# Performance work log

Hardware: AMD Instinct MI355X
Metric: run time of the kernel (lower is better)

## Reference

```python
import jax, jax.numpy as jnp
import numpy as np

B, P, D = 256, 256, 514          # batch, num_patches (16^2), model_dim
H, HD = 8, 64                    # n_heads, head_dim ((D-2)//H)
SH = 256                         # shared_hidden = head_mlp_hidden_dims[0]
HH = 256                         # per-head hidden (head_mlp_hidden_dims[1])
DFF = 2048                       # ffn hidden
LH = 2 * SH                      # lat_modulator hidden = shared_hidden*2
LD = D - 2                       # learnable_dim

def gelu(x):
    return jax.nn.gelu(x, approximate=False)  # torch nn.GELU default is exact erf

def setup_inputs() -> dict:
    key = jax.random.key(0)
    ks = jax.random.split(key, 16)
    s = 0.02
    x = jax.random.normal(ks[0], (B, P, D), dtype=jnp.float32)
    # shared spatial layer: Linear(P -> SH), torch weight layout [out, in]
    Ws = jax.random.normal(ks[1], (SH, P), dtype=jnp.float32) * s
    bs = jax.random.normal(ks[2], (SH,), dtype=jnp.float32) * s
    # lat modulator: Linear(2 -> LH), GELU, Linear(LH -> 2*SH) with special init
    LW1 = jax.random.normal(ks[3], (LH, 2), dtype=jnp.float32) * s
    Lb1 = jax.random.normal(ks[4], (LH,), dtype=jnp.float32) * s
    LW2 = jnp.zeros((2 * SH, LH), dtype=jnp.float32)  # zeroed per module init
    Lb2 = jnp.concatenate([jnp.ones((SH,), jnp.float32), jnp.zeros((SH,), jnp.float32)])
    # per-head processing: Linear(SH->HH), GELU, Linear(HH->P), stacked over heads
    HW1 = jax.random.normal(ks[5], (H, HH, SH), dtype=jnp.float32) * s
    Hb1 = jax.random.normal(ks[6], (H, HH), dtype=jnp.float32) * s
    HW2 = jax.random.normal(ks[7], (H, P, HH), dtype=jnp.float32) * s
    Hb2 = jax.random.normal(ks[8], (H, P), dtype=jnp.float32) * s
    # ffn: Linear(D -> DFF) with last-2 input cols zeroed, GELU, Linear(DFF -> LD)
    FW1 = jax.random.normal(ks[9], (DFF, D), dtype=jnp.float32) * s
    FW1 = FW1.at[:, -2:].set(0.0)
    Fb1 = jax.random.normal(ks[10], (DFF,), dtype=jnp.float32) * s
    FW2 = jax.random.normal(ks[11], (LD, DFF), dtype=jnp.float32) * s
    Fb2 = jax.random.normal(ks[12], (LD,), dtype=jnp.float32) * s
    return dict(x=x, Ws=Ws, bs=bs, LW1=LW1, Lb1=Lb1, LW2=LW2, Lb2=Lb2,
                HW1=HW1, Hb1=Hb1, HW2=HW2, Hb2=Hb2,
                FW1=FW1, Fb1=Fb1, FW2=FW2, Fb2=Fb2)

def reference(x, Ws, bs, LW1, Lb1, LW2, Lb2, HW1, Hb1, HW2, Hb2, FW1, Fb1, FW2, Fb2):
    central = P // 2
    sc_central = x[:, central, -2:]          # [B, 2]
    sc_all = x[:, :, -2:]                    # [B, P, 2]
    x_learn = x[:, :, :-2]                   # [B, P, LD]
    x_res = x_learn
    # all heads at once: [B, P, H, HD] -> [B, H, HD, P]
    xh = x_learn.reshape(B, P, H, HD).transpose(0, 2, 3, 1)
    shared = jnp.einsum('bhdp,op->bhdo', xh, Ws) + bs   # [B, H, HD, SH]
    # FiLM params (loop-invariant in original, hoisted here)
    mod = gelu(sc_central @ LW1.T + Lb1) @ LW2.T + Lb2  # [B, 2*SH]
    gamma = mod[:, :SH][:, None, None, :]
    beta = mod[:, SH:][:, None, None, :]
    shared = shared * gamma + beta
    # per-head MLPs as grouped GEMMs
    h = gelu(jnp.einsum('bhdo,hko->bhdk', shared, HW1) + Hb1[None, :, None, :])
    out = jnp.einsum('bhdk,hpk->bhdp', h, HW2) + Hb2[None, :, None, :]  # [B,H,HD,P]
    x_learn = out.transpose(0, 3, 1, 2).reshape(B, P, LD) + x_res
    x_full = jnp.concatenate([x_learn, sc_all], axis=-1)  # [B, P, D]
    f = gelu(x_full @ FW1.T + Fb1) @ FW2.T + Fb2          # [B, P, LD]
    x_learn = f + x_learn
    return jnp.concatenate([x_learn, sc_all], axis=-1)
```

## Files before the change

kernel.cpp:

```cpp
#include <hip/hip_runtime.h>
#include <math.h>

typedef __attribute__((ext_vector_type(8))) __bf16 bf16x8;
typedef __attribute__((ext_vector_type(4))) float f32x4;
typedef __attribute__((ext_vector_type(2))) float f32x2;

#define DEV __device__ __forceinline__

typedef __attribute__((address_space(3))) unsigned int lds_u32;
typedef __attribute__((address_space(1))) unsigned int glb_u32;

DEV unsigned short f2bf(float f) {
    unsigned int u = __builtin_bit_cast(unsigned int, f);
    u += 0x7FFFu + ((u >> 16) & 1u);
    return (unsigned short)(u >> 16);
}
DEV float bf2f(unsigned short u) {
    unsigned int v = (unsigned int)u << 16;
    return __builtin_bit_cast(float, v);
}
DEV unsigned int pack2(float a, float b) {
    return (unsigned int)f2bf(a) | ((unsigned int)f2bf(b) << 16);
}
DEV float gelu_exact(float v) {
    return 0.5f * v * (1.0f + erff(v * 0.70710678118654752f));
}
DEV float gelu_fast(float x) {
    float z = 1.5957691216f * x + 0.0713548163f * x * x * x;
    float e = __expf(-z);
    return x * __builtin_amdgcn_rcpf(1.0f + e);
}

__global__ void cast_bf16_kernel(const float* __restrict__ src,
                                 unsigned short* __restrict__ dst, int n) {
    int i = blockIdx.x * 256 + threadIdx.x;
    if (i < n) dst[i] = f2bf(src[i]);
}

__global__ void cast_fw1_kernel(const float* __restrict__ src,
                                unsigned short* __restrict__ dst) {
    int i = blockIdx.x * 256 + threadIdx.x;
    if (i < 2048 * 512) {
        int row = i >> 9, k = i & 511;
        dst[i] = f2bf(src[row * 514 + k]);
    }
}

__global__ void gb_kernel(const float* __restrict__ x,
                          const float* __restrict__ LW1, const float* __restrict__ Lb1,
                          const float* __restrict__ LW2, const float* __restrict__ Lb2,
                          float* __restrict__ gb) {
    __shared__ float t[8][512];
    const int b0 = blockIdx.x * 8, tid = threadIdx.x;
    for (int idx = tid; idx < 8 * 512; idx += 256) {
        int bb = idx >> 9, j = idx & 511;
        float s0 = x[((size_t)(b0 + bb) * 256 + 128) * 514 + 512];
        float s1 = x[((size_t)(b0 + bb) * 256 + 128) * 514 + 513];
        t[bb][j] = gelu_exact(LW1[j * 2] * s0 + LW1[j * 2 + 1] * s1 + Lb1[j]);
    }
    __syncthreads();
    const int i = tid;
    float a0[8], a1[8];
    float l0 = Lb2[i], l1 = Lb2[i + 256];
    #pragma unroll
    for (int bb = 0; bb < 8; ++bb) { a0[bb] = l0; a1[bb] = l1; }
    for (int j = 0; j < 512; ++j) {
        float w0 = LW2[(size_t)i * 512 + j];
        float w1 = LW2[(size_t)(i + 256) * 512 + j];
        #pragma unroll
        for (int bb = 0; bb < 8; ++bb) {
            a0[bb] += w0 * t[bb][j];
            a1[bb] += w1 * t[bb][j];
        }
    }
    #pragma unroll
    for (int bb = 0; bb < 8; ++bb) {
        gb[(size_t)(b0 + bb) * 512 + i] = a0[bb];
        gb[(size_t)(b0 + bb) * 512 + i + 256] = a1[bb];
    }
}

__global__ void sc_copy_kernel(const float* __restrict__ x, float* __restrict__ out,
                               float* __restrict__ scbuf) {
    size_t idx = (size_t)blockIdx.x * 256 + threadIdx.x;
    size_t off = idx * 514 + 512;
    f32x2 v = *(const f32x2*)(x + off);
    *(f32x2*)(out + off) = v;
    *(f32x2*)(scbuf + idx * 2) = v;
}

#define MPAD 264

__global__ __launch_bounds__(256, 2) void mixer_kernel(
    const float* __restrict__ x, const float* __restrict__ bs,
    const float* __restrict__ Hb1, const float* __restrict__ Hb2,
    const unsigned short* __restrict__ Wsb,
    const unsigned short* __restrict__ HW1b,
    const unsigned short* __restrict__ HW2b,
    const float* __restrict__ gb,
    unsigned short* __restrict__ Xb) {
    __shared__ __attribute__((aligned(16))) char smem[33792 + 34816];
    unsigned short* XT = (unsigned short*)smem;
    unsigned short* S = (unsigned short*)(smem + 33792);
    unsigned short* ST = S;

    const int bid = blockIdx.x;
    const int b = bid >> 3;
    const int h = bid & 7;
    const int tid = threadIdx.x;
    const int lane = tid & 63;
    const int w = tid >> 6;
    const int l15 = lane & 15;
    const int l4 = lane >> 4;

    {
        const int c = lane;
        const float* xp = x + ((size_t)b * 256) * 514 + (size_t)h * 64 + c;
        float v[64];
        #pragma unroll
        for (int p = 0; p < 64; ++p)
            v[p] = xp[(size_t)(w * 64 + p) * 514];
        #pragma unroll
        for (int g = 0; g < 8; ++g) {
            uint4 pk;
            pk.x = pack2(v[g * 8 + 0], v[g * 8 + 1]);
            pk.y = pack2(v[g * 8 + 2], v[g * 8 + 3]);
            pk.z = pack2(v[g * 8 + 4], v[g * 8 + 5]);
            pk.w = pack2(v[g * 8 + 6], v[g * 8 + 7]);
            *(uint4*)&XT[c * MPAD + w * 64 + g * 8] = pk;
        }
    }
    __syncthreads();

    f32x4 acc[4][4];

    #pragma unroll
    for (int mt = 0; mt < 4; ++mt)
        #pragma unroll
        for (int nt = 0; nt < 4; ++nt) acc[mt][nt] = 0.f;
    {
        const unsigned short* Wp = Wsb;
        bf16x8 bn1[4], bn2[4];
        #pragma unroll
        for (int nt = 0; nt < 4; ++nt) {
            bn1[nt] = *(const bf16x8*)(Wp + (size_t)(w * 64 + nt * 16 + l15) * 256 + 0 * 32 + l4 * 8);
            bn2[nt] = *(const bf16x8*)(Wp + (size_t)(w * 64 + nt * 16 + l15) * 256 + 1 * 32 + l4 * 8);
        }
        for (int kc = 0; kc < 8; ++kc) {
            bf16x8 bcur[4];
            #pragma unroll
            for (int nt = 0; nt < 4; ++nt) { bcur[nt] = bn1[nt]; bn1[nt] = bn2[nt]; }
            if (kc < 6) {
                #pragma unroll
                for (int nt = 0; nt < 4; ++nt)
                    bn2[nt] = *(const bf16x8*)(Wp + (size_t)(w * 64 + nt * 16 + l15) * 256 + (kc + 2) * 32 + l4 * 8);
            }
            #pragma unroll
            for (int mt = 0; mt < 4; ++mt) {
                bf16x8 afr = *(const bf16x8*)&XT[(mt * 16 + l15) * MPAD + kc * 32 + l4 * 8];
                #pragma unroll
                for (int nt = 0; nt < 4; ++nt)
                    acc[mt][nt] = __builtin_amdgcn_mfma_f32_16x16x32_bf16(afr, bcur[nt], acc[mt][nt], 0, 0, 0);
            }
        }
    }
    #pragma unroll
    for (int nt = 0; nt < 4; ++nt) {
        int o = w * 64 + nt * 16 + l15;
        float bsv = bs[o];
        float g = gb[(size_t)b * 512 + o];
        float be = gb[(size_t)b * 512 + 256 + o];
        #pragma unroll
        for (int mt = 0; mt < 4; ++mt)
            #pragma unroll
            for (int r = 0; r < 4; ++r) {
                int c = mt * 16 + l4 * 4 + r;
                S[c * MPAD + o] = f2bf((acc[mt][nt][r] + bsv) * g + be);
            }
    }
    __syncthreads();

    const unsigned short* W2p = HW1b + (size_t)h * 65536;
    #pragma unroll
    for (int mt = 0; mt < 4; ++mt)
        #pragma unroll
        for (int nt = 0; nt < 4; ++nt) acc[mt][nt] = 0.f;
    {
        bf16x8 bn1[4], bn2[4];
        #pragma unroll
        for (int nt = 0; nt < 4; ++nt) {
            bn1[nt] = *(const bf16x8*)(W2p + (size_t)(w * 64 + nt * 16 + l15) * 256 + 0 * 32 + l4 * 8);
            bn2[nt] = *(const bf16x8*)(W2p + (size_t)(w * 64 + nt * 16 + l15) * 256 + 1 * 32 + l4 * 8);
        }
        for (int kc = 0; kc < 8; ++kc) {
            bf16x8 bcur[4];
            #pragma unroll
            for (int nt = 0; nt < 4; ++nt) { bcur[nt] = bn1[nt]; bn1[nt] = bn2[nt]; }
            if (kc < 6) {
                #pragma unroll
                for (int nt = 0; nt < 4; ++nt)
                    bn2[nt] = *(const bf16x8*)(W2p + (size_t)(w * 64 + nt * 16 + l15) * 256 + (kc + 2) * 32 + l4 * 8);
            }
            #pragma unroll
            for (int mt = 0; mt < 4; ++mt) {
                bf16x8 afr = *(const bf16x8*)&S[(mt * 16 + l15) * MPAD + kc * 32 + l4 * 8];
                #pragma unroll
                for (int nt = 0; nt < 4; ++nt)
                    acc[mt][nt] = __builtin_amdgcn_mfma_f32_16x16x32_bf16(afr, bcur[nt], acc[mt][nt], 0, 0, 0);
            }
        }
    }
    __syncthreads();
    #pragma unroll
    for (int nt = 0; nt < 4; ++nt) {
        int kk = w * 64 + nt * 16 + l15;
        float hb = Hb1[(size_t)h * 256 + kk];
        #pragma unroll
        for (int mt = 0; mt < 4; ++mt)
            #pragma unroll
            for (int r = 0; r < 4; ++r) {
                int c = mt * 16 + l4 * 4 + r;
                S[c * MPAD + kk] = f2bf(gelu_fast(acc[mt][nt][r] + hb));
            }
    }
    __syncthreads();

    const unsigned short* W3p = HW2b + (size_t)h * 65536;
    #pragma unroll
    for (int mt = 0; mt < 4; ++mt)
        #pragma unroll
        for (int nt = 0; nt < 4; ++nt) acc[mt][nt] = 0.f;
    {
        bf16x8 bn1[4], bn2[4];
        #pragma unroll
        for (int nt = 0; nt < 4; ++nt) {
            bn1[nt] = *(const bf16x8*)(W3p + (size_t)(w * 64 + nt * 16 + l15) * 256 + 0 * 32 + l4 * 8);
            bn2[nt] = *(const bf16x8*)(W3p + (size_t)(w * 64 + nt * 16 + l15) * 256 + 1 * 32 + l4 * 8);
        }
        for (int kc = 0; kc < 8; ++kc) {
            bf16x8 bcur[4];
            #pragma unroll
            for (int nt = 0; nt < 4; ++nt) { bcur[nt] = bn1[nt]; bn1[nt] = bn2[nt]; }
            if (kc < 6) {
                #pragma unroll
                for (int nt = 0; nt < 4; ++nt)
                    bn2[nt] = *(const bf16x8*)(W3p + (size_t)(w * 64 + nt * 16 + l15) * 256 + (kc + 2) * 32 + l4 * 8);
            }
            #pragma unroll
            for (int mt = 0; mt < 4; ++mt) {
                bf16x8 afr = *(const bf16x8*)&S[(mt * 16 + l15) * MPAD + kc * 32 + l4 * 8];
                #pragma unroll
                for (int nt = 0; nt < 4; ++nt)
                    acc[mt][nt] = __builtin_amdgcn_mfma_f32_16x16x32_bf16(afr, bcur[nt], acc[mt][nt], 0, 0, 0);
            }
        }
    }
    __syncthreads();

    #pragma unroll
    for (int nt = 0; nt < 4; ++nt) {
        int p = w * 64 + nt * 16 + l15;
        float hb = Hb2[(size_t)h * 256 + p];
        #pragma unroll
        for (int mt = 0; mt < 4; ++mt) {
            int c0 = mt * 16 + l4 * 4;
            ushort4 uv;
            uv.x = f2bf(acc[mt][nt][0] + hb + bf2f(XT[(c0 + 0) * MPAD + p]));
            uv.y = f2bf(acc[mt][nt][1] + hb + bf2f(XT[(c0 + 1) * MPAD + p]));
            uv.z = f2bf(acc[mt][nt][2] + hb + bf2f(XT[(c0 + 2) * MPAD + p]));
            uv.w = f2bf(acc[mt][nt][3] + hb + bf2f(XT[(c0 + 3) * MPAD + p]));
            *(ushort4*)(ST + p * 68 + c0) = uv;
        }
    }
    __syncthreads();

    #pragma unroll
    for (int s = 0; s < 16; ++s) {
        int row = s * 16 + w * 4 + l4;
        ushort4 u = *(const ushort4*)(ST + row * 68 + l15 * 4);
        *(ushort4*)(Xb + ((size_t)(b * 256 + row)) * 512 + h * 64 + l15 * 4) = u;
    }
}

DEV void stage_m97(const unsigned short* g, size_t gstride, int row0, int k0,
                   char* lbuf, int tid) {
    const int slot = tid & 7;
    const int r8 = (tid >> 3) & 7;
    const int wv = tid >> 6;
    const int swz = (slot ^ r8) * 16;
    #pragma unroll
    for (int i = 0; i < 4; ++i) {
        int chunk = i * 4 + wv;
        int row = chunk * 8 + r8;
        const char* src = (const char*)(g + (size_t)(row0 + row) * gstride + k0) + swz;
        __builtin_amdgcn_global_load_lds((const glb_u32*)src,
                                         (lds_u32*)(lbuf + chunk * 1024), 16, 0, 0);
    }
}

DEV void gemm_loop97(const unsigned short* A, size_t sA,
                     const unsigned short* B, size_t sB,
                     int m0, int n0, int NT,
                     char* smem, int tid, f32x4 (&acc)[4][4]) {
    const int lane = tid & 63;
    const int w = tid >> 6;
    const int l15 = lane & 15, l4 = lane >> 4;
    const int wm = w >> 1, wn = w & 1;

    for (int t = 0; t < NT; ++t) {
        stage_m97(A, sA, m0, t * 64, smem, tid);
        stage_m97(B, sB, n0, t * 64, smem + 16384, tid);
        __syncthreads();
        #pragma unroll
        for (int kk = 0; kk < 2; ++kk) {
            bf16x8 af[4], bf[4];
            #pragma unroll
            for (int mf = 0; mf < 4; ++mf) {
                int row = wm * 64 + mf * 16 + l15;
                af[mf] = *(const bf16x8*)(smem + row * 128 + ((kk * 64 + l4 * 16) ^ ((row & 7) << 4)));
            }
            #pragma unroll
            for (int nf = 0; nf < 4; ++nf) {
                int row = wn * 64 + nf * 16 + l15;
                bf[nf] = *(const bf16x8*)(smem + 16384 + row * 128 + ((kk * 64 + l4 * 16) ^ ((row & 7) << 4)));
            }
            #pragma unroll
            for (int mf = 0; mf < 4; ++mf)
                #pragma unroll
                for (int nf = 0; nf < 4; ++nf)
                    acc[mf][nf] = __builtin_amdgcn_mfma_f32_16x16x32_bf16(
                        af[mf], bf[nf], acc[mf][nf], 0, 0, 0);
        }
        __syncthreads();
    }
}

__global__ __launch_bounds__(256, 3) void gemm1_kernel(
    const unsigned short* __restrict__ A,
    const unsigned short* __restrict__ B,
    const float* __restrict__ Fb1,
    const float* __restrict__ FW1,
    const float* __restrict__ scbuf,
    long pass_m0,
    unsigned short* __restrict__ G) {
    __shared__ __attribute__((aligned(16))) char smem[34816];

    const int nwg = gridDim.x;
    const int cpx = nwg >> 3;
    const int bid = (blockIdx.x & 7) * cpx + (blockIdx.x >> 3);
    const int m0 = (bid >> 4) * 128;
    const int n0 = (bid & 15) * 128;
    const int tid = threadIdx.x;
    const int lane = tid & 63;
    const int w = tid >> 6;
    const int l15 = lane & 15;
    const int l4 = lane >> 4;
    const int wm = w >> 1, wn = w & 1;

    f32x4 acc[4][4];
    #pragma unroll
    for (int mf = 0; mf < 4; ++mf)
        #pragma unroll
        for (int nf = 0; nf < 4; ++nf) acc[mf][nf] = 0.f;

    gemm_loop97(A, 512, B, 512, m0, n0, 8, smem, tid, acc);

    float fb[4], wa[4], wb[4];
    #pragma unroll
    for (int nf = 0; nf < 4; ++nf) {
        int n = n0 + wn * 64 + nf * 16 + l15;
        fb[nf] = Fb1[n];
        wa[nf] = FW1[(size_t)n * 514 + 512];
        wb[nf] = FW1[(size_t)n * 514 + 513];
    }
    f32x2 sc[4][4];
    #pragma unroll
    for (int mf = 0; mf < 4; ++mf)
        #pragma unroll
        for (int r = 0; r < 4; ++r) {
            long rowg = pass_m0 + m0 + wm * 64 + mf * 16 + l4 * 4 + r;
            sc[mf][r] = *(const f32x2*)(scbuf + rowg * 2);
        }
    unsigned short* LT = (unsigned short*)smem;
    #pragma unroll
    for (int mf = 0; mf < 4; ++mf)
        #pragma unroll
        for (int nf = 0; nf < 4; ++nf)
            #pragma unroll
            for (int r = 0; r < 4; ++r) {
                float v = acc[mf][nf][r] + fb[nf] + sc[mf][r].x * wa[nf] + sc[mf][r].y * wb[nf];
                int rl = wm * 64 + mf * 16 + l4 * 4 + r;
                LT[rl * 136 + wn * 64 + nf * 16 + l15] = f2bf(gelu_fast(v));
            }
    __syncthreads();
    {
        const int lane16 = tid & 15, rowq = tid >> 4;
        #pragma unroll
        for (int s = 0; s < 8; ++s) {
            int row = s * 16 + rowq;
            uint4 d = *(const uint4*)((const char*)smem + row * 272 + lane16 * 16);
            *(uint4*)(G + ((size_t)(m0 + row)) * 2048 + n0 + lane16 * 8) = d;
        }
    }
}

__global__ __launch_bounds__(256, 3) void gemm2_kernel(
    const unsigned short* __restrict__ A,
    const unsigned short* __restrict__ B,
    const float* __restrict__ Fb2,
    const unsigned short* __restrict__ Xb,
    long pass_m0,
    float* __restrict__ io) {
    __shared__ __attribute__((aligned(16))) char smem[32768];

    const int nwg = gridDim.x;
    const int cpx = nwg >> 3;
    const int bid = (blockIdx.x & 7) * cpx + (blockIdx.x >> 3);
    const int m0 = (bid >> 2) * 128;
    const int n0 = (bid & 3) * 128;
    const int tid = threadIdx.x;
    const int lane = tid & 63;
    const int w = tid >> 6;
    const int l15 = lane & 15;
    const int l4 = lane >> 4;
    const int wm = w >> 1, wn = w & 1;

    f32x4 acc[4][4];
    #pragma unroll
    for (int mf = 0; mf < 4; ++mf)
        #pragma unroll
        for (int nf = 0; nf < 4; ++nf) acc[mf][nf] = 0.f;

    gemm_loop97(A, 2048, B, 2048, m0, n0, 32, smem, tid, acc);

    #pragma unroll
    for (int nf = 0; nf < 4; ++nf) {
        int n = n0 + wn * 64 + nf * 16 + l15;
        float fbv = Fb2[n];
        #pragma unroll
        for (int mf = 0; mf < 4; ++mf)
            #pragma unroll
            for (int r = 0; r < 4; ++r) {
                long rowg = pass_m0 + m0 + wm * 64 + mf * 16 + l4 * 4 + r;
                float resv = bf2f(Xb[(size_t)rowg * 512 + n]);
                io[rowg * 514 + n] = acc[mf][nf][r] + fbv + resv;
            }
    }
}

extern "C" void kernel_launch(void* const* d_in, const int* in_sizes, int n_in,
                              void* d_out, int out_size, void* d_ws, size_t ws_size,
                              hipStream_t stream) {
    const float* x = (const float*)d_in[0];
    const float* Ws = (const float*)d_in[1];
    const float* bs = (const float*)d_in[2];
    const float* LW1 = (const float*)d_in[3];
    const float* Lb1 = (const float*)d_in[4];
    const float* LW2 = (const float*)d_in[5];
    const float* Lb2 = (const float*)d_in[6];
    const float* HW1 = (const float*)d_in[7];
    const float* Hb1 = (const float*)d_in[8];
    const float* HW2 = (const float*)d_in[9];
    const float* Hb2 = (const float*)d_in[10];
    const float* FW1 = (const float*)d_in[11];
    const float* Fb1 = (const float*)d_in[12];
    const float* FW2 = (const float*)d_in[13];
    const float* Fb2 = (const float*)d_in[14];
    float* out = (float*)d_out;

    char* ws = (char*)d_ws;
    unsigned short* Wsb = (unsigned short*)(ws);
    unsigned short* HW1b = (unsigned short*)(ws + 131072);
    unsigned short* HW2b = (unsigned short*)(ws + 1179648);
    unsigned short* FW1b = (unsigned short*)(ws + 2228224);
    unsigned short* FW2b = (unsigned short*)(ws + 4325376);
    float* gb = (float*)(ws + 6422528);
    float* scbuf = (float*)(ws + 6946816);
    unsigned short* Xb = (unsigned short*)(ws + 7471104);
    unsigned short* Gbuf = (unsigned short*)(ws + 7471104 + 67108864);

    const size_t fixed = 7471104 + 67108864;
    int npass = 32;
    for (int np = 2; np <= 32; np *= 2) {
        if (fixed + (size_t)268435456 / np <= ws_size) { npass = np; break; }
    }
    const long Mtot = 65536;
    const long Mp = Mtot / npass;

    cast_bf16_kernel<<<256, 256, 0, stream>>>(Ws, Wsb, 65536);
    cast_bf16_kernel<<<2048, 256, 0, stream>>>(HW1, HW1b, 524288);
    cast_bf16_kernel<<<2048, 256, 0, stream>>>(HW2, HW2b, 524288);
    cast_bf16_kernel<<<4096, 256, 0, stream>>>(FW2, FW2b, 1048576);
    cast_fw1_kernel<<<4096, 256, 0, stream>>>(FW1, FW1b);
    gb_kernel<<<32, 256, 0, stream>>>(x, LW1, Lb1, LW2, Lb2, gb);
    sc_copy_kernel<<<256, 256, 0, stream>>>(x, out, scbuf);

    mixer_kernel<<<2048, 256, 0, stream>>>(x, bs, Hb1, Hb2, Wsb, HW1b, HW2b, gb, Xb);

    for (int p = 0; p < npass; ++p) {
        long m0 = (long)p * Mp;
        gemm1_kernel<<<(int)(Mp / 128) * 16, 256, 0, stream>>>(
            Xb + m0 * 512, FW1b, Fb1, FW1, scbuf, m0, Gbuf);
        gemm2_kernel<<<(int)(Mp / 128) * 4, 256, 0, stream>>>(
            Gbuf, FW2b, Fb2, Xb, m0, out);
    }
}
```

Baseline: 594.1 us.

## Pre-transpose input to swizzled bf16 buffer and async-load it into mixer LDS

```diff
diff --git a/kernel.cpp b/kernel.cpp
--- a/kernel.cpp
+++ b/kernel.cpp
@@ -89,19 +89,57 @@
     *(f32x2*)(scbuf + idx * 2) = v;
 }
 
+__global__ void xt_kernel(const float* __restrict__ x,
+                          unsigned short* __restrict__ XTg) {
+    __shared__ float T[64 * 65];
+    const int bid = blockIdx.x;
+    const int b = bid >> 3, h = bid & 7;
+    const int tid = threadIdx.x;
+    char* outb = (char*)(XTg + ((size_t)(b * 8 + h)) * 16384);
+
+    for (int r = 0; r < 4; ++r) {
+        #pragma unroll
+        for (int j = 0; j < 8; ++j) {
+            int unit = j * 256 + tid;
+            int p = unit >> 5;
+            int cs = unit & 31;
+            f32x2 v = *(const f32x2*)(x + ((size_t)(b * 256 + r * 64 + p)) * 514 + h * 64 + cs * 2);
+            T[(cs * 2) * 65 + p] = v.x;
+            T[(cs * 2 + 1) * 65 + p] = v.y;
+        }
+        __syncthreads();
+        #pragma unroll
+        for (int j = 0; j < 2; ++j) {
+            int unit = j * 256 + tid;
+            int c = unit >> 3;
+            int seg = unit & 7;
+            const float* src = &T[c * 65 + seg * 8];
+            uint4 pk;
+            pk.x = pack2(src[0], src[1]);
+            pk.y = pack2(src[2], src[3]);
+            pk.z = pack2(src[4], src[5]);
+            pk.w = pack2(src[6], src[7]);
+            int off = (r * 128 + seg * 16) ^ ((c & 7) << 4);
+            *(uint4*)(outb + c * 512 + off) = pk;
+        }
+        __syncthreads();
+    }
+}
+
 #define MPAD 264
 
 __global__ __launch_bounds__(256, 2) void mixer_kernel(
-    const float* __restrict__ x, const float* __restrict__ bs,
+    const float* __restrict__ bs,
     const float* __restrict__ Hb1, const float* __restrict__ Hb2,
     const unsigned short* __restrict__ Wsb,
     const unsigned short* __restrict__ HW1b,
     const unsigned short* __restrict__ HW2b,
     const float* __restrict__ gb,
+    const unsigned short* __restrict__ XTg,
     unsigned short* __restrict__ Xb) {
-    __shared__ __attribute__((aligned(16))) char smem[33792 + 34816];
-    unsigned short* XT = (unsigned short*)smem;
-    unsigned short* S = (unsigned short*)(smem + 33792);
+    __shared__ __attribute__((aligned(16))) char smem[32768 + 34816];
+    char* XTb = smem;
+    unsigned short* S = (unsigned short*)(smem + 32768);
     unsigned short* ST = S;
 
     const int bid = blockIdx.x;
@@ -114,20 +152,12 @@
     const int l4 = lane >> 4;
 
     {
-        const int c = lane;
-        const float* xp = x + ((size_t)b * 256) * 514 + (size_t)h * 64 + c;
-        float v[64];
-        #pragma unroll
-        for (int p = 0; p < 64; ++p)
-            v[p] = xp[(size_t)(w * 64 + p) * 514];
-        #pragma unroll
-        for (int g = 0; g < 8; ++g) {
-            uint4 pk;
-            pk.x = pack2(v[g * 8 + 0], v[g * 8 + 1]);
-            pk.y = pack2(v[g * 8 + 2], v[g * 8 + 3]);
-            pk.z = pack2(v[g * 8 + 4], v[g * 8 + 5]);
-            pk.w = pack2(v[g * 8 + 6], v[g * 8 + 7]);
-            *(uint4*)&XT[c * MPAD + w * 64 + g * 8] = pk;
+        const char* XTgp = (const char*)(XTg + ((size_t)(b * 8 + h)) * 16384);
+        #pragma unroll
+        for (int i = 0; i < 8; ++i) {
+            int chunk = i * 4 + w;
+            __builtin_amdgcn_global_load_lds((const glb_u32*)(XTgp + chunk * 1024 + lane * 16),
+                                             (lds_u32*)(XTb + chunk * 1024), 16, 0, 0);
         }
     }
     __syncthreads();
@@ -157,7 +187,8 @@
             }
             #pragma unroll
             for (int mt = 0; mt < 4; ++mt) {
-                bf16x8 afr = *(const bf16x8*)&XT[(mt * 16 + l15) * MPAD + kc * 32 + l4 * 8];
+                int row = mt * 16 + l15;
+                bf16x8 afr = *(const bf16x8*)(XTb + row * 512 + ((kc * 64 + l4 * 16) ^ ((row & 7) << 4)));
                 #pragma unroll
                 for (int nt = 0; nt < 4; ++nt)
                     acc[mt][nt] = __builtin_amdgcn_mfma_f32_16x16x32_bf16(afr, bcur[nt], acc[mt][nt], 0, 0, 0);
@@ -265,10 +296,13 @@
         for (int mt = 0; mt < 4; ++mt) {
             int c0 = mt * 16 + l4 * 4;
             ushort4 uv;
-            uv.x = f2bf(acc[mt][nt][0] + hb + bf2f(XT[(c0 + 0) * MPAD + p]));
-            uv.y = f2bf(acc[mt][nt][1] + hb + bf2f(XT[(c0 + 1) * MPAD + p]));
-            uv.z = f2bf(acc[mt][nt][2] + hb + bf2f(XT[(c0 + 2) * MPAD + p]));
-            uv.w = f2bf(acc[mt][nt][3] + hb + bf2f(XT[(c0 + 3) * MPAD + p]));
+            #pragma unroll
+            for (int r = 0; r < 4; ++r) {
+                int c = c0 + r;
+                float xv = bf2f(*(const unsigned short*)(XTb + c * 512 + ((2 * p) ^ ((c & 7) << 4))));
+                float ov = acc[mt][nt][r] + hb + xv;
+                ((unsigned short*)&uv)[r] = f2bf(ov);
+            }
             *(ushort4*)(ST + p * 68 + c0) = uv;
         }
     }
@@ -477,9 +511,10 @@
     float* gb = (float*)(ws + 6422528);
     float* scbuf = (float*)(ws + 6946816);
     unsigned short* Xb = (unsigned short*)(ws + 7471104);
-    unsigned short* Gbuf = (unsigned short*)(ws + 7471104 + 67108864);
-
-    const size_t fixed = 7471104 + 67108864;
+    unsigned short* XTg = (unsigned short*)(ws + 7471104 + 67108864);
+    unsigned short* Gbuf = (unsigned short*)(ws + 7471104 + 134217728);
+
+    const size_t fixed = 7471104 + 134217728;
     int npass = 32;
     for (int np = 2; np <= 32; np *= 2) {
         if (fixed + (size_t)268435456 / np <= ws_size) { npass = np; break; }
@@ -494,8 +529,9 @@
     cast_fw1_kernel<<<4096, 256, 0, stream>>>(FW1, FW1b);
     gb_kernel<<<32, 256, 0, stream>>>(x, LW1, Lb1, LW2, Lb2, gb);
     sc_copy_kernel<<<256, 256, 0, stream>>>(x, out, scbuf);
-
-    mixer_kernel<<<2048, 256, 0, stream>>>(x, bs, Hb1, Hb2, Wsb, HW1b, HW2b, gb, Xb);
+    xt_kernel<<<2048, 256, 0, stream>>>(x, XTg);
+
+    mixer_kernel<<<2048, 256, 0, stream>>>(bs, Hb1, Hb2, Wsb, HW1b, HW2b, gb, XTg, Xb);
 
     for (int p = 0; p < npass; ++p) {
         long m0 = (long)p * Mp;
```

Result: slower. 619.4 us (+4.3%).

## Use 256x256 tiles with 8 waves and double-buffered staged FFN GEMM pipeline

Applied to the files above, without the earlier changes.

```diff
diff --git a/kernel.cpp b/kernel.cpp
--- a/kernel.cpp
+++ b/kernel.cpp
@@ -282,60 +282,137 @@
     }
 }
 
-DEV void stage_m97(const unsigned short* g, size_t gstride, int row0, int k0,
-                   char* lbuf, int tid) {
-    const int slot = tid & 7;
-    const int r8 = (tid >> 3) & 7;
-    const int wv = tid >> 6;
+DEV void stage_half8(const unsigned short* g, size_t gstride, int row0, int k0,
+                     char* half_base, int w, int lane) {
+    const int slot = lane & 7;
+    const int r8 = lane >> 3;
     const int swz = (slot ^ r8) * 16;
     #pragma unroll
-    for (int i = 0; i < 4; ++i) {
-        int chunk = i * 4 + wv;
+    for (int i = 0; i < 2; ++i) {
+        int chunk = w * 2 + i;
         int row = chunk * 8 + r8;
         const char* src = (const char*)(g + (size_t)(row0 + row) * gstride + k0) + swz;
         __builtin_amdgcn_global_load_lds((const glb_u32*)src,
-                                         (lds_u32*)(lbuf + chunk * 1024), 16, 0, 0);
-    }
-}
-
-DEV void gemm_loop97(const unsigned short* A, size_t sA,
-                     const unsigned short* B, size_t sB,
-                     int m0, int n0, int NT,
-                     char* smem, int tid, f32x4 (&acc)[4][4]) {
-    const int lane = tid & 63;
-    const int w = tid >> 6;
+                                         (lds_u32*)(half_base + chunk * 1024), 16, 0, 0);
+    }
+}
+
+#define FENCE() asm volatile("" ::: "memory")
+
+DEV void gemm_loop8(const unsigned short* A, size_t sA,
+                    const unsigned short* B, size_t sB,
+                    int m0, int n0, int NT,
+                    char* smem, int w, int lane, f32x4 (&acc)[8][4]) {
+    const int wm = w >> 2, wn = w & 3;
     const int l15 = lane & 15, l4 = lane >> 4;
-    const int wm = w >> 1, wn = w & 1;
-
-    for (int t = 0; t < NT; ++t) {
-        stage_m97(A, sA, m0, t * 64, smem, tid);
-        stage_m97(B, sB, n0, t * 64, smem + 16384, tid);
-        __syncthreads();
+    const int koff0 = (l4 * 16) ^ ((l15 & 7) << 4);
+    const int koff1 = (64 + l4 * 16) ^ ((l15 & 7) << 4);
+
+    stage_half8(A, sA, m0, 0, smem, w, lane);
+    stage_half8(A, sA, m0 + 128, 0, smem + 16384, w, lane);
+    stage_half8(B, sB, n0, 0, smem + 65536, w, lane);
+    stage_half8(B, sB, n0 + 128, 0, smem + 65536 + 16384, w, lane);
+    stage_half8(A, sA, m0, 64, smem + 32768, w, lane);
+    stage_half8(A, sA, m0 + 128, 64, smem + 32768 + 16384, w, lane);
+
+    for (int T = 0; T < NT; ++T) {
+        const int cb = T & 1;
+        const char* Ab = smem + cb * 32768;
+        const char* Bb = smem + 65536 + cb * 32768;
+        const int nbuf = cb ^ 1;
+
+        if (T + 1 < NT)
+            stage_half8(B, sB, n0, (T + 1) * 64, smem + 65536 + nbuf * 32768, w, lane);
+        if (T == NT - 1) asm volatile("s_waitcnt vmcnt(0)" ::: "memory");
+        else             asm volatile("s_waitcnt vmcnt(6)" ::: "memory");
+        __builtin_amdgcn_s_barrier();
+        FENCE();
+
+        bf16x8 Bf[2][4], Alo[2][4], Ahi[2][4];
         #pragma unroll
         for (int kk = 0; kk < 2; ++kk) {
-            bf16x8 af[4], bf[4];
-            #pragma unroll
-            for (int mf = 0; mf < 4; ++mf) {
-                int row = wm * 64 + mf * 16 + l15;
-                af[mf] = *(const bf16x8*)(smem + row * 128 + ((kk * 64 + l4 * 16) ^ ((row & 7) << 4)));
-            }
+            const int ko = kk ? koff1 : koff0;
             #pragma unroll
             for (int nf = 0; nf < 4; ++nf) {
                 int row = wn * 64 + nf * 16 + l15;
-                bf[nf] = *(const bf16x8*)(smem + 16384 + row * 128 + ((kk * 64 + l4 * 16) ^ ((row & 7) << 4)));
-            }
-            #pragma unroll
-            for (int mf = 0; mf < 4; ++mf)
+                Bf[kk][nf] = *(const bf16x8*)(Bb + row * 128 + ko);
+            }
+            #pragma unroll
+            for (int mf = 0; mf < 4; ++mf) {
+                int row = wm * 128 + mf * 16 + l15;
+                Alo[kk][mf] = *(const bf16x8*)(Ab + row * 128 + ko);
+            }
+        }
+        __builtin_amdgcn_s_setprio(1);
+        #pragma unroll
+        for (int kk = 0; kk < 2; ++kk)
+            #pragma unroll
+            for (int mf = 0; mf < 2; ++mf)
                 #pragma unroll
                 for (int nf = 0; nf < 4; ++nf)
                     acc[mf][nf] = __builtin_amdgcn_mfma_f32_16x16x32_bf16(
-                        af[mf], bf[nf], acc[mf][nf], 0, 0, 0);
-        }
-        __syncthreads();
-    }
-}
-
-__global__ __launch_bounds__(256, 3) void gemm1_kernel(
+                        Alo[kk][mf], Bf[kk][nf], acc[mf][nf], 0, 0, 0);
+        __builtin_amdgcn_s_setprio(0);
+        __builtin_amdgcn_s_barrier();
+        FENCE();
+
+        if (T + 1 < NT)
+            stage_half8(B, sB, n0 + 128, (T + 1) * 64, smem + 65536 + nbuf * 32768 + 16384, w, lane);
+        #pragma unroll
+        for (int kk = 0; kk < 2; ++kk) {
+            const int ko = kk ? koff1 : koff0;
+            #pragma unroll
+            for (int mf = 0; mf < 4; ++mf) {
+                int row = wm * 128 + (mf + 4) * 16 + l15;
+                Ahi[kk][mf] = *(const bf16x8*)(Ab + row * 128 + ko);
+            }
+        }
+        __builtin_amdgcn_s_setprio(1);
+        #pragma unroll
+        for (int kk = 0; kk < 2; ++kk)
+            #pragma unroll
+            for (int mf = 2; mf < 4; ++mf)
+                #pragma unroll
+                for (int nf = 0; nf < 4; ++nf)
+                    acc[mf][nf] = __builtin_amdgcn_mfma_f32_16x16x32_bf16(
+                        Alo[kk][mf], Bf[kk][nf], acc[mf][nf], 0, 0, 0);
+        __builtin_amdgcn_s_setprio(0);
+        __builtin_amdgcn_s_barrier();
+        FENCE();
+
+        if (T + 2 < NT)
+            stage_half8(A, sA, m0, (T + 2) * 64, smem + cb * 32768, w, lane);
+        __builtin_amdgcn_s_setprio(1);
+        #pragma unroll
+        for (int kk = 0; kk < 2; ++kk)
+            #pragma unroll
+            for (int mf = 0; mf < 2; ++mf)
+                #pragma unroll
+                for (int nf = 0; nf < 4; ++nf)
+                    acc[mf + 4][nf] = __builtin_amdgcn_mfma_f32_16x16x32_bf16(
+                        Ahi[kk][mf], Bf[kk][nf], acc[mf + 4][nf], 0, 0, 0);
+        __builtin_amdgcn_s_setprio(0);
+        __builtin_amdgcn_s_barrier();
+        FENCE();
+
+        if (T + 2 < NT)
+            stage_half8(A, sA, m0 + 128, (T + 2) * 64, smem + cb * 32768 + 16384, w, lane);
+        __builtin_amdgcn_s_setprio(1);
+        #pragma unroll
+        for (int kk = 0; kk < 2; ++kk)
+            #pragma unroll
+            for (int mf = 2; mf < 4; ++mf)
+                #pragma unroll
+                for (int nf = 0; nf < 4; ++nf)
+                    acc[mf + 4][nf] = __builtin_amdgcn_mfma_f32_16x16x32_bf16(
+                        Ahi[kk][mf], Bf[kk][nf], acc[mf + 4][nf], 0, 0, 0);
+        __builtin_amdgcn_s_setprio(0);
+        __builtin_amdgcn_s_barrier();
+        FENCE();
+    }
+}
+
+__global__ __launch_bounds__(512, 1) void gemm1_kernel(
     const unsigned short* __restrict__ A,
     const unsigned short* __restrict__ B,
     const float* __restrict__ Fb1,
@@ -343,27 +420,29 @@
     const float* __restrict__ scbuf,
     long pass_m0,
     unsigned short* __restrict__ G) {
-    __shared__ __attribute__((aligned(16))) char smem[34816];
+    __shared__ __attribute__((aligned(16))) char smem[131072];
 
     const int nwg = gridDim.x;
     const int cpx = nwg >> 3;
     const int bid = (blockIdx.x & 7) * cpx + (blockIdx.x >> 3);
-    const int m0 = (bid >> 4) * 128;
-    const int n0 = (bid & 15) * 128;
+    const int m0 = (bid >> 3) * 256;
+    const int n0 = (bid & 7) * 256;
     const int tid = threadIdx.x;
     const int lane = tid & 63;
     const int w = tid >> 6;
     const int l15 = lane & 15;
     const int l4 = lane >> 4;
-    const int wm = w >> 1, wn = w & 1;
-
-    f32x4 acc[4][4];
-    #pragma unroll
-    for (int mf = 0; mf < 4; ++mf)
+    const int wm = w >> 2, wn = w & 3;
+
+    f32x4 acc[8][4];
+    #pragma unroll
+    for (int mf = 0; mf < 8; ++mf)
         #pragma unroll
         for (int nf = 0; nf < 4; ++nf) acc[mf][nf] = 0.f;
 
-    gemm_loop97(A, 512, B, 512, m0, n0, 8, smem, tid, acc);
+    gemm_loop8(A, 512, B, 512, m0, n0, 8, smem, w, lane, acc);
+    __builtin_amdgcn_s_barrier();
+    FENCE();
 
     float fb[4], wa[4], wb[4];
     #pragma unroll
@@ -373,77 +452,82 @@
         wa[nf] = FW1[(size_t)n * 514 + 512];
         wb[nf] = FW1[(size_t)n * 514 + 513];
     }
-    f32x2 sc[4][4];
-    #pragma unroll
-    for (int mf = 0; mf < 4; ++mf)
-        #pragma unroll
-        for (int r = 0; r < 4; ++r) {
-            long rowg = pass_m0 + m0 + wm * 64 + mf * 16 + l4 * 4 + r;
-            sc[mf][r] = *(const f32x2*)(scbuf + rowg * 2);
-        }
     unsigned short* LT = (unsigned short*)smem;
     #pragma unroll
-    for (int mf = 0; mf < 4; ++mf)
-        #pragma unroll
-        for (int nf = 0; nf < 4; ++nf)
-            #pragma unroll
-            for (int r = 0; r < 4; ++r) {
-                float v = acc[mf][nf][r] + fb[nf] + sc[mf][r].x * wa[nf] + sc[mf][r].y * wb[nf];
-                int rl = wm * 64 + mf * 16 + l4 * 4 + r;
-                LT[rl * 136 + wn * 64 + nf * 16 + l15] = f2bf(gelu_fast(v));
-            }
-    __syncthreads();
-    {
-        const int lane16 = tid & 15, rowq = tid >> 4;
-        #pragma unroll
-        for (int s = 0; s < 8; ++s) {
-            int row = s * 16 + rowq;
-            uint4 d = *(const uint4*)((const char*)smem + row * 272 + lane16 * 16);
-            *(uint4*)(G + ((size_t)(m0 + row)) * 2048 + n0 + lane16 * 8) = d;
-        }
-    }
-}
-
-__global__ __launch_bounds__(256, 3) void gemm2_kernel(
+    for (int ph = 0; ph < 2; ++ph) {
+        if (wm == ph) {
+            #pragma unroll
+            for (int mfg = 0; mfg < 8; ++mfg) {
+                f32x2 sc[4];
+                #pragma unroll
+                for (int r = 0; r < 4; ++r) {
+                    long rowg = pass_m0 + m0 + ph * 128 + mfg * 16 + l4 * 4 + r;
+                    sc[r] = *(const f32x2*)(scbuf + rowg * 2);
+                }
+                #pragma unroll
+                for (int nf = 0; nf < 4; ++nf)
+                    #pragma unroll
+                    for (int r = 0; r < 4; ++r) {
+                        float v = acc[mfg][nf][r] + fb[nf] + sc[r].x * wa[nf] + sc[r].y * wb[nf];
+                        int rl = mfg * 16 + l4 * 4 + r;
+                        LT[rl * 264 + wn * 64 + nf * 16 + l15] = f2bf(gelu_fast(v));
+                    }
+            }
+        }
+        __syncthreads();
+        {
+            const int row16 = tid >> 5, col16 = tid & 31;
+            #pragma unroll
+            for (int sp = 0; sp < 8; ++sp) {
+                int row = sp * 16 + row16;
+                uint4 d = *(const uint4*)((const char*)smem + row * 528 + col16 * 16);
+                *(uint4*)(G + ((size_t)(m0 + ph * 128 + row)) * 2048 + n0 + col16 * 8) = d;
+            }
+        }
+        __syncthreads();
+    }
+}
+
+__global__ __launch_bounds__(512, 1) void gemm2_kernel(
     const unsigned short* __restrict__ A,
     const unsigned short* __restrict__ B,
     const float* __restrict__ Fb2,
     const unsigned short* __restrict__ Xb,
     long pass_m0,
     float* __restrict__ io) {
-    __shared__ __attribute__((aligned(16))) char smem[32768];
+    __shared__ __attribute__((aligned(16))) char smem[131072];
 
     const int nwg = gridDim.x;
     const int cpx = nwg >> 3;
     const int bid = (blockIdx.x & 7) * cpx + (blockIdx.x >> 3);
-    const int m0 = (bid >> 2) * 128;
-    const int n0 = (bid & 3) * 128;
+    const int m0 = (bid >> 1) * 256;
+    const int n0 = (bid & 1) * 256;
     const int tid = threadIdx.x;
     const int lane = tid & 63;
     const int w = tid >> 6;
     const int l15 = lane & 15;
     const int l4 = lane >> 4;
-    const int wm = w >> 1, wn = w & 1;
-
-    f32x4 acc[4][4];
-    #pragma unroll
-    for (int mf = 0; mf < 4; ++mf)
+    const int wm = w >> 2, wn = w & 3;
+
+    f32x4 acc[8][4];
+    #pragma unroll
+    for (int mf = 0; mf < 8; ++mf)
         #pragma unroll
         for (int nf = 0; nf < 4; ++nf) acc[mf][nf] = 0.f;
 
-    gemm_loop97(A, 2048, B, 2048, m0, n0, 32, smem, tid, acc);
+    gemm_loop8(A, 2048, B, 2048, m0, n0, 32, smem, w, lane, acc);
 
     #pragma unroll
     for (int nf = 0; nf < 4; ++nf) {
         int n = n0 + wn * 64 + nf * 16 + l15;
         float fbv = Fb2[n];
         #pragma unroll
-        for (int mf = 0; mf < 4; ++mf)
+        for (int mfg = 0; mfg < 8; ++mfg)
             #pragma unroll
             for (int r = 0; r < 4; ++r) {
-                long rowg = pass_m0 + m0 + wm * 64 + mf * 16 + l4 * 4 + r;
+                long rowg = pass_m0 + m0 + wm * 128 + mfg * 16 + l4 * 4 + r;
                 float resv = bf2f(Xb[(size_t)rowg * 512 + n]);
-                io[rowg * 514 + n] = acc[mf][nf][r] + fbv + resv;
+                io[rowg * 514 + n] = acc[mfg][nf][r] + fbv + resv;
             }
     }
 }
@@ -499,9 +583,9 @@
 
     for (int p = 0; p < npass; ++p) {
         long m0 = (long)p * Mp;
-        gemm1_kernel<<<(int)(Mp / 128) * 16, 256, 0, stream>>>(
+        gemm1_kernel<<<(int)(Mp / 256) * 8, 512, 0, stream>>>(
             Xb + m0 * 512, FW1b, Fb1, FW1, scbuf, m0, Gbuf);
-        gemm2_kernel<<<(int)(Mp / 128) * 4, 256, 0, stream>>>(
+        gemm2_kernel<<<(int)(Mp / 256) * 2, 512, 0, stream>>>(
             Gbuf, FW2b, Fb2, Xb, m0, out);
     }
 }
```

New measurement: 637.9 us. 7.4% more time.
